# Optimization experiments

Measured on AMD Instinct MI355X. Metric: run time of the kernel, lower is better.

## Reference

```python
import jax, jax.numpy as jnp
import numpy as np
import math

B, S, E = 4, 1024, 1024
H = 16
HD = E // H            # 64
HD2 = HD // 2          # 32
DEPTH = 12 - 1
LAMBDA_INIT = 0.8 - 0.6 * math.exp(-0.3 * DEPTH)
EPS = 1e-5


def setup_inputs() -> dict:
    key = jax.random.key(0)
    ks = jax.random.split(key, 16)
    std = 1.0 / math.sqrt(E)
    inp = {
        "hidden_states": jax.random.normal(ks[0], (B, S, E), jnp.float32),
        "q_w": jax.random.normal(ks[1], (E, E), jnp.float32) * std,
        "q_b": jnp.zeros((E,), jnp.float32),
        "k_w": jax.random.normal(ks[2], (E, E), jnp.float32) * std,
        "k_b": jnp.zeros((E,), jnp.float32),
        "v_w": jax.random.normal(ks[3], (E, E), jnp.float32) * std,
        "v_b": jnp.zeros((E,), jnp.float32),
        "o_w": jax.random.normal(ks[4], (E, E), jnp.float32) * std,
        "o_b": jnp.zeros((E,), jnp.float32),
        "lambda_q1": jax.random.normal(ks[5], (HD2,), jnp.float32) * 0.1,
        "lambda_k1": jax.random.normal(ks[6], (HD2,), jnp.float32) * 0.1,
        "lambda_q2": jax.random.normal(ks[7], (HD2,), jnp.float32) * 0.1,
        "lambda_k2": jax.random.normal(ks[8], (HD2,), jnp.float32) * 0.1,
        "subln_w": jnp.ones((HD,), jnp.float32),
    }
    return inp


def reference(hidden_states, q_w, q_b, k_w, k_b, v_w, v_b, o_w, o_b,
              lambda_q1, lambda_k1, lambda_q2, lambda_k2, subln_w):
    b, s, _ = hidden_states.shape
    # projections (torch Linear: x @ W.T + b)
    q = hidden_states @ q_w.T + q_b
    k = hidden_states @ k_w.T + k_b
    v = hidden_states @ v_w.T + v_b
    # split q/k into 2*H heads of dim HD2; v into H heads of dim HD
    q = q.reshape(b, s, 2 * H, HD2).transpose(0, 2, 1, 3)   # [B,2H,S,HD2]
    k = k.reshape(b, s, 2 * H, HD2).transpose(0, 2, 1, 3)   # [B,2H,S,HD2]
    v = v.reshape(b, s, H, HD).transpose(0, 2, 1, 3)        # [B,H,S,HD]
    # scores scaled by sqrt(head_dim) (full head_dim, per source)
    scores = jnp.einsum('bhqd,bhkd->bhqk', q, k) / math.sqrt(HD)
    scores = jnp.nan_to_num(scores)
    attn_w = jax.nn.softmax(scores.astype(jnp.float32), axis=-1).astype(scores.dtype)
    lam1 = jnp.exp(jnp.sum(lambda_q1 * lambda_k1))
    lam2 = jnp.exp(jnp.sum(lambda_q2 * lambda_k2))
    lam = lam1 - lam2 + LAMBDA_INIT
    attn_w = attn_w.reshape(b, H, 2, s, s)
    diff_w = attn_w[:, :, 0] - lam * attn_w[:, :, 1]        # [B,H,S,S]
    attn = jnp.einsum('bhqk,bhkd->bhqd', diff_w, v)          # [B,H,S,HD]
    # RMSNorm over head dim, elementwise affine
    attn = attn * jax.lax.rsqrt(jnp.mean(attn * attn, axis=-1, keepdims=True) + EPS) * subln_w
    attn = attn * (1.0 - LAMBDA_INIT)
    attn = attn.transpose(0, 2, 1, 3).reshape(b, s, H * HD)
    out = attn @ o_w.T + o_b
    return out, diff_w
```

## Files before the change

### kernel.cpp

```cpp
#include <hip/hip_runtime.h>

typedef __attribute__((ext_vector_type(8))) short short8;
typedef __attribute__((ext_vector_type(4))) float floatx4;

#define MFMA16(a, b, c) __builtin_amdgcn_mfma_f32_16x16x32_bf16((a), (b), (c), 0, 0, 0)

#define LAMBDA_INIT_F 0.777870099559256f
#define ONE_MINUS_LAMBDA_F 0.222129900440744f

#define GLL(g, l)                                                              \
  __builtin_amdgcn_global_load_lds(                                            \
      (const __attribute__((address_space(1))) void*)(g),                      \
      (__attribute__((address_space(3))) void*)(l), 16, 0, 0)

static __device__ __forceinline__ unsigned short f2bf(float f) {
  union { float f; unsigned int u; } v; v.f = f;
  unsigned int r = v.u + 0x7FFFu + ((v.u >> 16) & 1u);
  return (unsigned short)(r >> 16);
}

__global__ __launch_bounds__(256) void cvt_f32_bf16(const float* __restrict__ in,
                                                    unsigned short* __restrict__ out,
                                                    int n4) {
  int i = blockIdx.x * 256 + threadIdx.x;
  if (i < n4) {
    float4 v = ((const float4*)in)[i];
    unsigned short o0 = f2bf(v.x), o1 = f2bf(v.y), o2 = f2bf(v.z), o3 = f2bf(v.w);
    ushort2 a = {o0, o1}, b = {o2, o3};
    ((ushort2*)out)[i * 2] = a;
    ((ushort2*)out)[i * 2 + 1] = b;
  }
}

__device__ __forceinline__ void gemm128_core(const unsigned short* __restrict__ A,
                                             const unsigned short* __restrict__ Bt,
                                             unsigned short* As, unsigned short* Bs,
                                             int m0, int n0, floatx4 (&acc)[4][4]) {
  const int tid = threadIdx.x;
  const int w = tid >> 6, lane = tid & 63;
  const int lrow = lane & 15, quad = lane >> 4;
  const int wm = (w >> 1) * 64, wn = (w & 1) * 64;

#pragma unroll
  for (int i = 0; i < 4; i++)
#pragma unroll
    for (int j = 0; j < 4; j++)
      acc[i][j] = (floatx4){0.f, 0.f, 0.f, 0.f};

  const int ar = tid >> 2;
  const int ac = (tid & 3) * 8;
  const unsigned short* ga = A + (size_t)(m0 + ar) * 1024 + ac;
  const unsigned short* gb = Bt + (size_t)(n0 + ar) * 1024 + ac;
  unsigned short* la = As + w * 512;
  unsigned short* lb = Bs + w * 512;

  for (int k0 = 0; k0 < 1024; k0 += 32) {
    GLL(ga + k0, la);
    GLL(ga + k0 + 64 * 1024, la + 2048);
    GLL(gb + k0, lb);
    GLL(gb + k0 + 64 * 1024, lb + 2048);
    __syncthreads();
    short8 af[4], bfr[4];
#pragma unroll
    for (int i = 0; i < 4; i++)
      af[i] = *(const short8*)(As + (wm + i * 16 + lrow) * 32 + quad * 8);
#pragma unroll
    for (int j = 0; j < 4; j++)
      bfr[j] = *(const short8*)(Bs + (wn + j * 16 + lrow) * 32 + quad * 8);
#pragma unroll
    for (int i = 0; i < 4; i++)
#pragma unroll
      for (int j = 0; j < 4; j++)
        acc[i][j] = MFMA16(af[i], bfr[j], acc[i][j]);
    __syncthreads();
  }
}

__global__ __launch_bounds__(256, 2) void gemm_qkv(const unsigned short* __restrict__ A,
                                                   const unsigned short* __restrict__ qw,
                                                   const unsigned short* __restrict__ kw,
                                                   const unsigned short* __restrict__ vw,
                                                   const float* __restrict__ qb,
                                                   const float* __restrict__ kb,
                                                   const float* __restrict__ vb,
                                                   unsigned short* __restrict__ qh,
                                                   unsigned short* __restrict__ kh,
                                                   unsigned short* __restrict__ vnat) {
  __shared__ unsigned short As[128 * 32];
  __shared__ unsigned short Bs[128 * 32];
  const int m0 = blockIdx.y * 128;
  const int nglob = blockIdx.x * 128;
  const int wsel = nglob >> 10;
  const int nloc = nglob & 1023;
  const unsigned short* Bt = (wsel == 0) ? qw : ((wsel == 1) ? kw : vw);
  const float* bias = (wsel == 0) ? qb : ((wsel == 1) ? kb : vb);

  floatx4 acc[4][4];
  gemm128_core(A, Bt, As, Bs, m0, nloc, acc);

  const int tid = threadIdx.x;
  const int w = tid >> 6, lane = tid & 63;
  const int lrow = lane & 15, quad = lane >> 4;
  const int wm = (w >> 1) * 64, wn = (w & 1) * 64;

#pragma unroll
  for (int i = 0; i < 4; i++)
#pragma unroll
    for (int j = 0; j < 4; j++) {
      int col = nloc + wn + j * 16 + lrow;
      float bcol = bias[col];
#pragma unroll
      for (int r = 0; r < 4; r++) {
        int row = m0 + wm + i * 16 + quad * 4 + r;
        float v = acc[i][j][r] + bcol;
        if (wsel < 2) {
          int b = row >> 10, s = row & 1023, h2 = col >> 5, d = col & 31;
          unsigned short* o = (wsel == 0) ? qh : kh;
          o[((((size_t)(b * 32 + h2)) << 10) + s) * 32 + d] = f2bf(v);
        } else {
          vnat[(size_t)row * 1024 + col] = f2bf(v);
        }
      }
    }
}

__global__ __launch_bounds__(256, 2) void gemm_o(const unsigned short* __restrict__ A,
                                                 const unsigned short* __restrict__ ow,
                                                 const float* __restrict__ ob,
                                                 float* __restrict__ out) {
  __shared__ unsigned short As[128 * 32];
  __shared__ unsigned short Bs[128 * 32];
  const int m0 = blockIdx.y * 128;
  const int n0 = blockIdx.x * 128;

  floatx4 acc[4][4];
  gemm128_core(A, ow, As, Bs, m0, n0, acc);

  const int tid = threadIdx.x;
  const int w = tid >> 6, lane = tid & 63;
  const int lrow = lane & 15, quad = lane >> 4;
  const int wm = (w >> 1) * 64, wn = (w & 1) * 64;

#pragma unroll
  for (int i = 0; i < 4; i++)
#pragma unroll
    for (int j = 0; j < 4; j++) {
      int col = n0 + wn + j * 16 + lrow;
      float bcol = ob[col];
#pragma unroll
      for (int r = 0; r < 4; r++) {
        int row = m0 + wm + i * 16 + quad * 4 + r;
        out[(size_t)row * 1024 + col] = acc[i][j][r] + bcol;
      }
    }
}

__global__ __launch_bounds__(256) void transpose_v(const unsigned short* __restrict__ vn,
                                                   unsigned short* __restrict__ vt) {
  __shared__ unsigned int tile[64][65];
  const int t = threadIdx.x;
  const int bh = blockIdx.y, b = bh >> 4, h = bh & 15;
  const int s0 = blockIdx.x * 64;
#pragma unroll
  for (int i = 0; i < 2; i++) {
    int r = i * 32 + (t >> 3);
    int c8 = (t & 7) * 8;
    short8 v = *(const short8*)(vn + ((size_t)(b * 1024 + s0 + r)) * 1024 + h * 64 + c8);
#pragma unroll
    for (int j = 0; j < 8; j++) tile[r][c8 + j] = (unsigned short)v[j];
  }
  __syncthreads();
  const int w = t >> 6, lane = t & 63;
#pragma unroll
  for (int dd = 0; dd < 16; dd++) {
    int d = w * 16 + dd;
    unsigned short u = (unsigned short)tile[lane][d];
    vt[(((size_t)(b * 16 + h)) * 64 + d) * 1024 + s0 + lane] = u;
  }
}

__global__ __launch_bounds__(256) void attn_fused(const unsigned short* __restrict__ qh,
                                                  const unsigned short* __restrict__ kh,
                                                  const unsigned short* __restrict__ vt,
                                                  const float* __restrict__ lq1,
                                                  const float* __restrict__ lk1,
                                                  const float* __restrict__ lq2,
                                                  const float* __restrict__ lk2,
                                                  const float* __restrict__ subln,
                                                  float* __restrict__ diffw,
                                                  unsigned short* __restrict__ attnb) {
  __shared__ unsigned short dsA[4][16][40];
  __shared__ float dsF[4][16][68];

  const int tid = threadIdx.x;
  const int w = tid >> 6, lane = tid & 63;
  const int lrow = lane & 15, quad = lane >> 4;
  const int chunk = blockIdx.x * 4 + w;
  const int cidx = chunk & 63, bh = chunk >> 6;
  const int b = bh >> 4, h = bh & 15;
  const int r0 = cidx * 16;

  float sl1 = 0.f, sl2 = 0.f;
  for (int i = 0; i < 32; i++) { sl1 += lq1[i] * lk1[i]; sl2 += lq2[i] * lk2[i]; }
  const float lam = __expf(sl1) - __expf(sl2) + LAMBDA_INIT_F;

  const unsigned short* q1 = qh + ((((size_t)(b * 32 + 2 * h)) << 10) + r0) * 32;
  const unsigned short* q2 = q1 + (32u << 10);
  const unsigned short* k1 = kh + (((size_t)(b * 32 + 2 * h)) << 10) * 32;
  const unsigned short* k2 = k1 + (32u << 10);
  const unsigned short* vth = vt + (((size_t)(b * 16 + h)) << 16);

  short8 a1 = *(const short8*)(q1 + lrow * 32 + quad * 8);
  short8 a2 = *(const short8*)(q2 + lrow * 32 + quad * 8);

  const floatx4 zero = (floatx4){0.f, 0.f, 0.f, 0.f};

  float sum1[4] = {0.f, 0.f, 0.f, 0.f}, sum2[4] = {0.f, 0.f, 0.f, 0.f};
#pragma unroll 8
  for (int ct = 0; ct < 64; ct++) {
    short8 bk1 = *(const short8*)(k1 + (size_t)(ct * 16 + lrow) * 32 + quad * 8);
    short8 bk2 = *(const short8*)(k2 + (size_t)(ct * 16 + lrow) * 32 + quad * 8);
    floatx4 s1 = MFMA16(a1, bk1, zero);
    floatx4 s2 = MFMA16(a2, bk2, zero);
#pragma unroll
    for (int r = 0; r < 4; r++) {
      sum1[r] += __expf(s1[r] * 0.125f);
      sum2[r] += __expf(s2[r] * 0.125f);
    }
  }
#pragma unroll
  for (int off = 1; off < 16; off <<= 1)
#pragma unroll
    for (int r = 0; r < 4; r++) {
      sum1[r] += __shfl_xor(sum1[r], off);
      sum2[r] += __shfl_xor(sum2[r], off);
    }
  float il1[4], il2[4];
#pragma unroll
  for (int r = 0; r < 4; r++) {
    il1[r] = 1.f / sum1[r];
    il2[r] = lam / sum2[r];
  }

  floatx4 accO[4];
#pragma unroll
  for (int nt = 0; nt < 4; nt++) accO[nt] = zero;

  float* dwbase = diffw + (((size_t)bh) << 20) + (size_t)r0 * 1024;

  for (int c4 = 0; c4 < 16; c4++) {
#pragma unroll
    for (int half = 0; half < 2; half++) {
#pragma unroll
      for (int cc = 0; cc < 2; cc++) {
        int ct = c4 * 4 + half * 2 + cc;
        short8 bk1 = *(const short8*)(k1 + (size_t)(ct * 16 + lrow) * 32 + quad * 8);
        short8 bk2 = *(const short8*)(k2 + (size_t)(ct * 16 + lrow) * 32 + quad * 8);
        floatx4 s1 = MFMA16(a1, bk1, zero);
        floatx4 s2 = MFMA16(a2, bk2, zero);
#pragma unroll
        for (int r = 0; r < 4; r++) {
          float p1 = __expf(s1[r] * 0.125f) * il1[r];
          float p2 = __expf(s2[r] * 0.125f) * il2[r];
          float d = p1 - p2;
          dsF[w][quad * 4 + r][half * 32 + cc * 16 + lrow] = d;
          dsA[w][quad * 4 + r][cc * 16 + lrow] = f2bf(d);
        }
      }
      short8 ad = *(const short8*)(&dsA[w][lrow][quad * 8]);
#pragma unroll
      for (int nt = 0; nt < 4; nt++) {
        short8 bv = *(const short8*)(vth + (size_t)(nt * 16 + lrow) * 1024 +
                                     (c4 * 2 + half) * 32 + quad * 8);
        accO[nt] = MFMA16(ad, bv, accO[nt]);
      }
    }
#pragma unroll
    for (int i = 0; i < 4; i++) {
      int rr = i * 4 + quad;
      floatx4 vv = *(const floatx4*)&dsF[w][rr][lrow * 4];
      __builtin_nontemporal_store(vv,
          (floatx4*)(dwbase + (size_t)rr * 1024 + c4 * 64 + lrow * 4));
    }
  }

#pragma unroll
  for (int r = 0; r < 4; r++) {
    float ss = 0.f;
#pragma unroll
    for (int nt = 0; nt < 4; nt++) ss += accO[nt][r] * accO[nt][r];
#pragma unroll
    for (int off = 1; off < 16; off <<= 1) ss += __shfl_xor(ss, off);
    float rs = rsqrtf(ss * (1.f / 64.f) + 1e-5f);
    int row = r0 + quad * 4 + r;
#pragma unroll
    for (int nt = 0; nt < 4; nt++) {
      float v = accO[nt][r] * rs * subln[nt * 16 + lrow] * ONE_MINUS_LAMBDA_F;
      attnb[((((size_t)b) << 10) + row) * 1024 + h * 64 + nt * 16 + lrow] = f2bf(v);
    }
  }
}

extern "C" void kernel_launch(void* const* d_in, const int* in_sizes, int n_in,
                              void* d_out, int out_size, void* d_ws, size_t ws_size,
                              hipStream_t stream) {
  (void)in_sizes; (void)n_in; (void)out_size; (void)ws_size;
  const float* hs = (const float*)d_in[0];
  const float* q_w = (const float*)d_in[1];
  const float* q_b = (const float*)d_in[2];
  const float* k_w = (const float*)d_in[3];
  const float* k_b = (const float*)d_in[4];
  const float* v_w = (const float*)d_in[5];
  const float* v_b = (const float*)d_in[6];
  const float* o_w = (const float*)d_in[7];
  const float* o_b = (const float*)d_in[8];
  const float* lq1 = (const float*)d_in[9];
  const float* lk1 = (const float*)d_in[10];
  const float* lq2 = (const float*)d_in[11];
  const float* lk2 = (const float*)d_in[12];
  const float* subln = (const float*)d_in[13];

  char* ws = (char*)d_ws;
  unsigned short* hs_bf = (unsigned short*)(ws + 0);
  unsigned short* attnb = (unsigned short*)(ws + 0);
  unsigned short* qw_bf = (unsigned short*)(ws + 8388608);
  unsigned short* kw_bf = (unsigned short*)(ws + 10485760);
  unsigned short* vw_bf = (unsigned short*)(ws + 12582912);
  unsigned short* ow_bf = (unsigned short*)(ws + 14680064);
  unsigned short* q_h = (unsigned short*)(ws + 16777216);
  unsigned short* k_h = (unsigned short*)(ws + 25165824);
  unsigned short* v_nat = (unsigned short*)(ws + 33554432);
  unsigned short* v_t = (unsigned short*)(ws + 41943040);

  cvt_f32_bf16<<<4096, 256, 0, stream>>>(hs, hs_bf, 1048576);
  cvt_f32_bf16<<<1024, 256, 0, stream>>>(q_w, qw_bf, 262144);
  cvt_f32_bf16<<<1024, 256, 0, stream>>>(k_w, kw_bf, 262144);
  cvt_f32_bf16<<<1024, 256, 0, stream>>>(v_w, vw_bf, 262144);
  cvt_f32_bf16<<<1024, 256, 0, stream>>>(o_w, ow_bf, 262144);

  gemm_qkv<<<dim3(24, 32), 256, 0, stream>>>(hs_bf, qw_bf, kw_bf, vw_bf,
                                             q_b, k_b, v_b, q_h, k_h, v_nat);

  transpose_v<<<dim3(16, 64), 256, 0, stream>>>(v_nat, v_t);

  float* outf = (float*)d_out;
  attn_fused<<<1024, 256, 0, stream>>>(q_h, k_h, v_t, lq1, lk1, lq2, lk2, subln,
                                       outf + 4194304, attnb);

  gemm_o<<<dim3(8, 32), 256, 0, stream>>>(attnb, ow_bf, o_b, outf);
}
```

Before: 478.2 us.

## Fuse V transpose into QKV GEMM epilogue and batch weight conversions

The QKV GEMM epilogue now stages each 32-column slice of the output tile in shared memory and writes Q/K head-major and V pre-transposed with 16-byte vector stores. This removes the separate transpose_v kernel and the v_nat intermediate buffer. The output GEMM epilogue is also staged through LDS so it can issue coalesced float4 stores. The four weight-conversion launches are merged into one 2D-grid launch. The cost is extra LDS traffic and barriers in the epilogues.

```diff
diff --git a/kernel.cpp b/kernel.cpp
--- a/kernel.cpp
+++ b/kernel.cpp
@@ -32,6 +32,24 @@
   }
 }
 
+__global__ __launch_bounds__(256) void cvt_w4(const float* __restrict__ a,
+                                              const float* __restrict__ b,
+                                              const float* __restrict__ c,
+                                              const float* __restrict__ d,
+                                              unsigned short* __restrict__ oa,
+                                              unsigned short* __restrict__ ob,
+                                              unsigned short* __restrict__ oc,
+                                              unsigned short* __restrict__ od) {
+  int sel = blockIdx.y;
+  const float* in = (sel == 0) ? a : (sel == 1) ? b : (sel == 2) ? c : d;
+  unsigned short* out = (sel == 0) ? oa : (sel == 1) ? ob : (sel == 2) ? oc : od;
+  int i = blockIdx.x * 256 + threadIdx.x;
+  float4 v = ((const float4*)in)[i];
+  ushort2 x = {f2bf(v.x), f2bf(v.y)}, y = {f2bf(v.z), f2bf(v.w)};
+  ((ushort2*)out)[i * 2] = x;
+  ((ushort2*)out)[i * 2 + 1] = y;
+}
+
 __device__ __forceinline__ void gemm128_core(const unsigned short* __restrict__ A,
                                              const unsigned short* __restrict__ Bt,
                                              unsigned short* As, unsigned short* Bs,
@@ -85,9 +103,8 @@
                                                    const float* __restrict__ vb,
                                                    unsigned short* __restrict__ qh,
                                                    unsigned short* __restrict__ kh,
-                                                   unsigned short* __restrict__ vnat) {
-  __shared__ unsigned short As[128 * 32];
-  __shared__ unsigned short Bs[128 * 32];
+                                                   unsigned short* __restrict__ vt) {
+  __shared__ unsigned short SMEM[8192];
   const int m0 = blockIdx.y * 128;
   const int nglob = blockIdx.x * 128;
   const int wsel = nglob >> 10;
@@ -96,86 +113,105 @@
   const float* bias = (wsel == 0) ? qb : ((wsel == 1) ? kb : vb);
 
   floatx4 acc[4][4];
-  gemm128_core(A, Bt, As, Bs, m0, nloc, acc);
+  gemm128_core(A, Bt, SMEM, SMEM + 4096, m0, nloc, acc);
 
   const int tid = threadIdx.x;
   const int w = tid >> 6, lane = tid & 63;
   const int lrow = lane & 15, quad = lane >> 4;
-  const int wm = (w >> 1) * 64, wn = (w & 1) * 64;
-
-#pragma unroll
-  for (int i = 0; i < 4; i++)
-#pragma unroll
-    for (int j = 0; j < 4; j++) {
-      int col = nloc + wn + j * 16 + lrow;
-      float bcol = bias[col];
-#pragma unroll
-      for (int r = 0; r < 4; r++) {
-        int row = m0 + wm + i * 16 + quad * 4 + r;
-        float v = acc[i][j][r] + bcol;
-        if (wsel < 2) {
-          int b = row >> 10, s = row & 1023, h2 = col >> 5, d = col & 31;
-          unsigned short* o = (wsel == 0) ? qh : kh;
-          o[((((size_t)(b * 32 + h2)) << 10) + s) * 32 + d] = f2bf(v);
-        } else {
-          vnat[(size_t)row * 1024 + col] = f2bf(v);
-        }
-      }
-    }
+  const int wm = (w >> 1) * 64;
+  const int bb = m0 >> 10;
+  const int sbase = m0 & 1023;
+
+  for (int p = 0; p < 4; p++) {
+    if ((w & 1) == (p >> 1)) {
+      const int jbase = (p & 1) * 2;
+#pragma unroll
+      for (int jj = 0; jj < 2; jj++) {
+        const int j = jbase + jj;
+        const int lcol = jj * 16 + lrow;
+        const float bcol = bias[nloc + p * 32 + lcol];
+#pragma unroll
+        for (int i = 0; i < 4; i++)
+#pragma unroll
+          for (int r = 0; r < 4; r++) {
+            const int row = wm + i * 16 + quad * 4 + r;
+            unsigned short bv = f2bf(acc[i][j][r] + bcol);
+            if (wsel < 2)
+              SMEM[row * 32 + lcol] = bv;
+            else
+              SMEM[lcol * 136 + row] = bv;
+          }
+      }
+    }
+    __syncthreads();
+    if (wsel < 2) {
+      const int h2 = (nloc + p * 32) >> 5;
+      unsigned short* o = ((wsel == 0) ? qh : kh) +
+                          ((((size_t)(bb * 32 + h2)) << 10) + sbase) * 32;
+#pragma unroll
+      for (int inst = 0; inst < 8; inst++) {
+        int idx = inst * 512 + lane * 8;
+        *(short8*)(o + idx) = *(const short8*)(SMEM + idx);
+      }
+    } else {
+      const int gcol = nloc + p * 32;
+      const int h = gcol >> 6, d0 = gcol & 63;
+      unsigned short* o = vt + ((((size_t)(bb * 16 + h)) * 64 + d0) * 1024) + sbase;
+#pragma unroll
+      for (int inst = 0; inst < 8; inst++) {
+        int col = inst * 4 + (lane >> 4);
+        int sr = (lane & 15) * 8;
+        *(short8*)(o + (size_t)col * 1024 + sr) =
+            *(const short8*)(SMEM + col * 136 + sr);
+      }
+    }
+    __syncthreads();
+  }
 }
 
 __global__ __launch_bounds__(256, 2) void gemm_o(const unsigned short* __restrict__ A,
                                                  const unsigned short* __restrict__ ow,
                                                  const float* __restrict__ ob,
                                                  float* __restrict__ out) {
-  __shared__ unsigned short As[128 * 32];
-  __shared__ unsigned short Bs[128 * 32];
+  __shared__ unsigned short SMEM[8192];
   const int m0 = blockIdx.y * 128;
   const int n0 = blockIdx.x * 128;
 
   floatx4 acc[4][4];
-  gemm128_core(A, ow, As, Bs, m0, n0, acc);
+  gemm128_core(A, ow, SMEM, SMEM + 4096, m0, n0, acc);
 
   const int tid = threadIdx.x;
   const int w = tid >> 6, lane = tid & 63;
   const int lrow = lane & 15, quad = lane >> 4;
-  const int wm = (w >> 1) * 64, wn = (w & 1) * 64;
-
-#pragma unroll
-  for (int i = 0; i < 4; i++)
-#pragma unroll
-    for (int j = 0; j < 4; j++) {
-      int col = n0 + wn + j * 16 + lrow;
-      float bcol = ob[col];
-#pragma unroll
-      for (int r = 0; r < 4; r++) {
-        int row = m0 + wm + i * 16 + quad * 4 + r;
-        out[(size_t)row * 1024 + col] = acc[i][j][r] + bcol;
-      }
-    }
-}
-
-__global__ __launch_bounds__(256) void transpose_v(const unsigned short* __restrict__ vn,
-                                                   unsigned short* __restrict__ vt) {
-  __shared__ unsigned int tile[64][65];
-  const int t = threadIdx.x;
-  const int bh = blockIdx.y, b = bh >> 4, h = bh & 15;
-  const int s0 = blockIdx.x * 64;
-#pragma unroll
-  for (int i = 0; i < 2; i++) {
-    int r = i * 32 + (t >> 3);
-    int c8 = (t & 7) * 8;
-    short8 v = *(const short8*)(vn + ((size_t)(b * 1024 + s0 + r)) * 1024 + h * 64 + c8);
-#pragma unroll
-    for (int j = 0; j < 8; j++) tile[r][c8 + j] = (unsigned short)v[j];
-  }
-  __syncthreads();
-  const int w = t >> 6, lane = t & 63;
-#pragma unroll
-  for (int dd = 0; dd < 16; dd++) {
-    int d = w * 16 + dd;
-    unsigned short u = (unsigned short)tile[lane][d];
-    vt[(((size_t)(b * 16 + h)) * 64 + d) * 1024 + s0 + lane] = u;
+  const int wm = (w >> 1) * 64;
+  float* SF = (float*)SMEM;
+
+  for (int p = 0; p < 4; p++) {
+    if ((w & 1) == (p >> 1)) {
+      const int jbase = (p & 1) * 2;
+#pragma unroll
+      for (int jj = 0; jj < 2; jj++) {
+        const int j = jbase + jj;
+        const int lcol = jj * 16 + lrow;
+        const float bcol = ob[n0 + p * 32 + lcol];
+#pragma unroll
+        for (int i = 0; i < 4; i++)
+#pragma unroll
+          for (int r = 0; r < 4; r++) {
+            const int row = wm + i * 16 + quad * 4 + r;
+            SF[row * 32 + lcol] = acc[i][j][r] + bcol;
+          }
+      }
+    }
+    __syncthreads();
+#pragma unroll
+    for (int inst = 0; inst < 16; inst++) {
+      int row = inst * 8 + (lane >> 3);
+      int c4 = (lane & 7) * 4;
+      *(floatx4*)(out + (size_t)(m0 + row) * 1024 + n0 + p * 32 + c4) =
+          *(const floatx4*)(SF + row * 32 + c4);
+    }
+    __syncthreads();
   }
 }
 
@@ -329,19 +365,14 @@
   unsigned short* ow_bf = (unsigned short*)(ws + 14680064);
   unsigned short* q_h = (unsigned short*)(ws + 16777216);
   unsigned short* k_h = (unsigned short*)(ws + 25165824);
-  unsigned short* v_nat = (unsigned short*)(ws + 33554432);
   unsigned short* v_t = (unsigned short*)(ws + 41943040);
 
   cvt_f32_bf16<<<4096, 256, 0, stream>>>(hs, hs_bf, 1048576);
-  cvt_f32_bf16<<<1024, 256, 0, stream>>>(q_w, qw_bf, 262144);
-  cvt_f32_bf16<<<1024, 256, 0, stream>>>(k_w, kw_bf, 262144);
-  cvt_f32_bf16<<<1024, 256, 0, stream>>>(v_w, vw_bf, 262144);
-  cvt_f32_bf16<<<1024, 256, 0, stream>>>(o_w, ow_bf, 262144);
+  cvt_w4<<<dim3(1024, 4), 256, 0, stream>>>(q_w, k_w, v_w, o_w,
+                                            qw_bf, kw_bf, vw_bf, ow_bf);
 
   gemm_qkv<<<dim3(24, 32), 256, 0, stream>>>(hs_bf, qw_bf, kw_bf, vw_bf,
-                                             q_b, k_b, v_b, q_h, k_h, v_nat);
-
-  transpose_v<<<dim3(16, 64), 256, 0, stream>>>(v_nat, v_t);
+                                             q_b, k_b, v_b, q_h, k_h, v_t);
 
   float* outf = (float*)d_out;
   attn_fused<<<1024, 256, 0, stream>>>(q_h, k_h, v_t, lq1, lk1, lq2, lk2, subln,
```

After: 480.1 us. About the same (+0.4%).
